# Optimization experiments

Measured on AMD Instinct MI355X. Metric: run time of the kernel, lower is better.

Reference implementation:

```python
import jax, jax.numpy as jnp
import numpy as np
from jax import lax

B, C, T, D, H, W = 1, 8, 8, 24, 48, 48
KT = 3  # temporal kernel taps (module's time loop == valid forward conv, stride 1, pad 0)
KS = 3  # spatial kernel size
S = 2   # spatial stride of the transposed conv
P = 1   # spatial padding of the transposed conv


def setup_inputs() -> dict:
    key = jax.random.key(0)
    kx, kw = jax.random.split(key)
    x = jax.random.normal(kx, (B, C, T, D, H, W), dtype=jnp.float32)
    # torch layout (out_channels, in_channels, kT, kD, kH, kW); the module assigns the
    # slice weight[:, :, i] directly as ConvTranspose3d.weight, so at runtime dim0 acts
    # as the transpose-conv INPUT-channel dim (works because in_ch == out_ch).
    fan_in = C * KT * KS ** 3
    bound = float(1.0 / np.sqrt(fan_in))
    weight = jax.random.uniform(kw, (C, C, KT, KS, KS, KS), dtype=jnp.float32,
                                minval=-bound, maxval=bound)
    return {"x": x, "weight": weight}


def _convT3d(x5, wt):
    # x5: [N, Cin, D, H, W]; wt: ConvTranspose3d weight laid out [Cin, Cout, kD, kH, kW].
    # Transposed conv == forward conv with spatially flipped kernel, swapped I/O dims,
    # lhs dilation = stride, per-side padding = dil*(k-1) - p.
    rhs = jnp.flip(wt, axis=(2, 3, 4)).transpose(1, 0, 2, 3, 4)  # [Cout, Cin, k, k, k]
    pad = KS - 1 - P
    return lax.conv_general_dilated(
        x5, rhs,
        window_strides=(1, 1, 1),
        padding=[(pad, pad)] * 3,
        lhs_dilation=(S, S, S),
        dimension_numbers=("NCDHW", "OIDHW", "NCDHW"))


def reference(x, weight):
    b, c, t = x.shape[:3]
    t_o = t - (KT - 1)  # temporal valid forward conv: out[f] = sum_i conv_i(x[f + i])
    # fold time into batch so each temporal tap is a single big 3D conv
    xr = x.transpose(0, 2, 1, 3, 4, 5).reshape(b * t, c, *x.shape[3:])
    out = None
    for i in range(KT):  # small fixed loop over kernel taps
        y = _convT3d(xr, weight[:, :, i])                 # [b*t, C, Do, Ho, Wo]
        y = y.reshape(b, t, *y.shape[1:])[:, i:i + t_o]   # frames x[f+i] -> out[f]
        out = y if out is None else out + y
    return out.transpose(0, 2, 1, 3, 4, 5)  # [B, C, t_o, Do, Ho, Wo]
```

## Files before the change

kernel.cpp:

```cpp
#include <hip/hip_runtime.h>


typedef float  f32x4  __attribute__((ext_vector_type(4)));
typedef float  f4a    __attribute__((ext_vector_type(4)));
typedef short  bf16x8 __attribute__((ext_vector_type(8)));
typedef unsigned int u32;
typedef u32    u32x2  __attribute__((ext_vector_type(2)));
typedef u32    u32x4  __attribute__((ext_vector_type(4)));

namespace {
constexpr int T_ = 8, D_ = 24, H_ = 48, W_ = 48;
constexpr int TO = 6, DO_ = 47, HO = 95, WO = 95;
constexpr int XCS = T_ * D_ * H_ * W_;
constexpr int XFS = D_ * H_ * W_;
constexpr int XDS = H_ * W_;
constexpr long OCS = (long)TO * DO_ * HO * WO;
constexpr int OFS = DO_ * HO * WO;
constexpr int ODS = HO * WO;

constexpr int AG[4] = {24, 12, 12, 8};
constexpr int AOFF[4] = {0, 3072, 4608, 6144};
constexpr int NRSTR = 146;

__global__ __launch_bounds__(256) void pack_kernel(const float* __restrict__ w,
                                                   unsigned short* __restrict__ A) {
  const int tid = blockIdx.x * 256 + threadIdx.x;
  const int nthr = gridDim.x * 256;
  const int KR[4] = {192, 96, 96, 48};
  for (int c = 0; c < 4; ++c) {
    const int cnt = AG[c] * 128;
    for (int e = tid; e < cnt; e += nthr) {
      const int j = e & 7, r = (e >> 3) & 15, g = e >> 7;
      const int k = g * 8 + j;
      float v = 0.f;
      if (k < KR[c]) {
        int gg = -1, kd = 1, kh = 1;
        const int cc = j & 1;
        if (c == 0)      { gg = g;               kd = ((j >> 1) & 1) ? 2 : 0; kh = ((j >> 2) & 1) ? 0 : 2; }
        else if (c == 1) { gg = 2 * g + (j >> 2); kd = ((j >> 1) & 1) ? 2 : 0; kh = 1; }
        else if (c == 2) { gg = 2 * g + (j >> 2); kd = 1; kh = ((j >> 1) & 1) ? 0 : 2; }
        else             { gg = 4 * g + (j >> 1); kd = 1; kh = 1; }
        if (gg >= 0 && gg < 24) {
          const int ci = gg / 3, i = gg - 3 * (gg / 3);
          const int co = r & 7;
          int kw = (r < 8) ? (cc == 0 ? 1 : -1) : (cc == 0 ? 2 : 0);
          if (kw >= 0) v = w[ci * 648 + co * 81 + i * 27 + kd * 9 + kh * 3 + kw];
        }
      }
      u32 u = __float_as_uint(v);
      u += 0x7FFFu + ((u >> 16) & 1u);
      A[AOFF[c] + e] = (unsigned short)(u >> 16);
    }
  }
}

template<int PD, int PH>
__device__ __forceinline__ void wave_body(
    const u32* __restrict__ lds, const unsigned short* __restrict__ A,
    float* __restrict__ out, int f, int od, int oh, int ihb, int lane)
{
  constexpr int CLS = (PD && PH) ? 0 : PD ? 1 : PH ? 2 : 3;
  constexpr int NSTEP = (CLS == 0) ? 6 : (CLS == 3) ? 2 : 3;
  const int c15 = lane & 15, q = lane >> 4;
  const int th = ((oh + PH) >> 1) - ihb;

  bf16x8 af[NSTEP];
  {
    const unsigned short* Ap = A + AOFF[CLS] + c15 * 8;
    #pragma unroll
    for (int s = 0; s < NSTEP; ++s)
      af[s] = *reinterpret_cast<const bf16x8*>(Ap + (s * 4 + q) * 128);
  }

  f32x4 acc[3];
  #pragma unroll
  for (int b = 0; b < 3; ++b) acc[b] = {0, 0, 0, 0};

  #pragma unroll
  for (int blk = 0; blk < 3; ++blk) {
    const int n = blk * 16 + c15;
    const u32* col = lds + n * NRSTR;
    #pragma unroll
    for (int s = 0; s < NSTEP; ++s) {
      const int G = s * 4 + q;
      u32x4 ue;
      if constexpr (CLS == 0) {
        const u32* b = col + G * 6 + 2 * th - 2;
        const u32x2 lo = *reinterpret_cast<const u32x2*>(b);
        const u32x2 hi = *reinterpret_cast<const u32x2*>(b + 2);
        ue = u32x4{lo.x, lo.y, hi.x, hi.y};
      } else if constexpr (CLS == 1) {
        const u32* b = col + 2 * G * 6 + 2 * th;
        const u32x2 lo = *reinterpret_cast<const u32x2*>(b);
        const u32x2 hi = *reinterpret_cast<const u32x2*>(b + 6);
        ue = u32x4{lo.x, lo.y, hi.x, hi.y};
      } else if constexpr (CLS == 2) {
        const u32* b = col + 2 * G * 6 + 2 * th - 1;
        ue = u32x4{b[0], b[2], b[6], b[8]};
      } else {
        const int g4 = (G > 5) ? 20 : 4 * G;
        const u32* b = col + g4 * 6 + 2 * th + 1;
        ue = u32x4{b[0], b[6], b[12], b[18]};
      }
      acc[blk] = __builtin_amdgcn_mfma_f32_16x16x32_bf16(af[s], __builtin_bit_cast(bf16x8, ue), acc[blk], 0, 0, 0);
    }
  }

  const int isO = (q >= 2);
  const int co0 = (q & 1) * 4;
  #pragma unroll
  for (int blk = 0; blk < 3; ++blk) {
    const int ow = blk * 32 + 2 * c15 + isO;
    if (ow < 95) {
      const long ob = (long)f * OFS + (long)od * ODS + (long)oh * HO + ow;
      #pragma unroll
      for (int j = 0; j < 4; ++j)
        out[(long)(co0 + j) * OCS + ob] = acc[blk][j];
    }
  }
}

constexpr int NBLK = 6 * 24 * 24;

__global__ __launch_bounds__(512) void convt4d_kernel(
    const float* __restrict__ x, const unsigned short* __restrict__ A,
    float* __restrict__ out)
{
  __shared__ u32 lds[48 * NRSTR];

  constexpr int qq = NBLK / 8;
  const int bid = blockIdx.x;
  const int L = (bid & 7) * qq + (bid >> 3);
  const int og = L % 24;
  const int rest = L / 24;
  const int odp = rest % 24, f = rest / 24;

  const int tid = threadIdx.x;
  const int ihb = og * 2;
  const int idp = odp + 1;

  for (int c = tid; c < 144 * 12; c += 512) {
    const int row = c / 12, ch = c % 12;
    const int gg = row / 6;
    const int rem = row % 6;
    const int t = rem >> 1, e = rem & 1;
    const int i = gg % 3, ci = gg / 3;
    int plane = idp - e; if (plane > 23) plane = 23;
    int ih = ihb + t; if (ih > 47) ih = 47;
    const float* src = x + ci * XCS + (f + i) * XFS + plane * XDS + ih * W_ + ch * 4;
    const f4a v = *reinterpret_cast<const f4a*>(src);
    const float v4 = (ch == 11) ? 0.f : src[4];
    const u32 b0 = __float_as_uint(v.x), b1 = __float_as_uint(v.y);
    const u32 b2 = __float_as_uint(v.z), b3 = __float_as_uint(v.w);
    const u32 b4 = __float_as_uint(v4);
    u32* dst = lds + (4 * ch) * NRSTR + row;
    dst[0 * NRSTR] = __builtin_amdgcn_perm(b1, b0, 0x07060302u);
    dst[1 * NRSTR] = __builtin_amdgcn_perm(b2, b1, 0x07060302u);
    dst[2 * NRSTR] = __builtin_amdgcn_perm(b3, b2, 0x07060302u);
    dst[3 * NRSTR] = __builtin_amdgcn_perm(b4, b3, 0x07060302u);
  }
  __syncthreads();

  const int w = tid >> 6, lane = tid & 63;
  const int half = w >> 2;
  const int od = 2 * odp + half;
  if (od > 46) return;
  int oh = og * 4 + (w & 3);
  if (oh > 94) oh = 93;
  if (half) {
    if (oh & 1) wave_body<1, 1>(lds, A, out, f, od, oh, ihb, lane);
    else        wave_body<1, 0>(lds, A, out, f, od, oh, ihb, lane);
  } else {
    if (oh & 1) wave_body<0, 1>(lds, A, out, f, od, oh, ihb, lane);
    else        wave_body<0, 0>(lds, A, out, f, od, oh, ihb, lane);
  }
}
}

extern "C" void kernel_launch(void* const* d_in, const int* in_sizes, int n_in,
                              void* d_out, int out_size, void* d_ws, size_t ws_size,
                              hipStream_t stream) {
  const float* x = (const float*)d_in[0];
  const float* w = (const float*)d_in[1];
  float* out = (float*)d_out;
  unsigned short* A = (unsigned short*)d_ws;
  hipLaunchKernelGGL(pack_kernel, dim3(8), dim3(256), 0, stream, w, A);
  hipLaunchKernelGGL(convt4d_kernel, dim3(NBLK), dim3(512), 0, stream, x, A, out);
}
```

Baseline: 35.73 us.

## Compute two output frames per block to reuse staged input frames in LDS

Each block now produces two consecutive output time frames. It stages 4 input frames per channel in LDS (192 rows instead of 144), and the two frames share 2 of those staged input frames. The grid is halved and each wave keeps two accumulator sets. This cuts redundant global reads and LDS packing of overlapping temporal frames. In exchange it adds LDS per block, more registers and fewer blocks, which may lower occupancy and parallelism.

```diff
diff --git a/kernel.cpp b/kernel.cpp
--- a/kernel.cpp
+++ b/kernel.cpp
@@ -20,7 +20,7 @@
 
 constexpr int AG[4] = {24, 12, 12, 8};
 constexpr int AOFF[4] = {0, 3072, 4608, 6144};
-constexpr int NRSTR = 146;
+constexpr int NRSTR = 194;
 
 __global__ __launch_bounds__(256) void pack_kernel(const float* __restrict__ w,
                                                    unsigned short* __restrict__ A) {
@@ -54,10 +54,15 @@
   }
 }
 
+__device__ __forceinline__ int rowb(int gg, int dl) {
+  const int ci = gg / 3;
+  return (ci * 4 + (gg - 3 * ci) + dl) * 6;
+}
+
 template<int PD, int PH>
 __device__ __forceinline__ void wave_body(
     const u32* __restrict__ lds, const unsigned short* __restrict__ A,
-    float* __restrict__ out, int f, int od, int oh, int ihb, int lane)
+    float* __restrict__ out, int f0, int od, int oh, int ihb, int lane)
 {
   constexpr int CLS = (PD && PH) ? 0 : PD ? 1 : PH ? 2 : 3;
   constexpr int NSTEP = (CLS == 0) ? 6 : (CLS == 3) ? 2 : 3;
@@ -72,9 +77,11 @@
       af[s] = *reinterpret_cast<const bf16x8*>(Ap + (s * 4 + q) * 128);
   }
 
-  f32x4 acc[3];
+  f32x4 acc[2][3];
   #pragma unroll
-  for (int b = 0; b < 3; ++b) acc[b] = {0, 0, 0, 0};
+  for (int dl = 0; dl < 2; ++dl)
+    #pragma unroll
+    for (int b = 0; b < 3; ++b) acc[dl][b] = {0, 0, 0, 0};
 
   #pragma unroll
   for (int blk = 0; blk < 3; ++blk) {
@@ -83,44 +90,54 @@
     #pragma unroll
     for (int s = 0; s < NSTEP; ++s) {
       const int G = s * 4 + q;
-      u32x4 ue;
-      if constexpr (CLS == 0) {
-        const u32* b = col + G * 6 + 2 * th - 2;
-        const u32x2 lo = *reinterpret_cast<const u32x2*>(b);
-        const u32x2 hi = *reinterpret_cast<const u32x2*>(b + 2);
-        ue = u32x4{lo.x, lo.y, hi.x, hi.y};
-      } else if constexpr (CLS == 1) {
-        const u32* b = col + 2 * G * 6 + 2 * th;
-        const u32x2 lo = *reinterpret_cast<const u32x2*>(b);
-        const u32x2 hi = *reinterpret_cast<const u32x2*>(b + 6);
-        ue = u32x4{lo.x, lo.y, hi.x, hi.y};
-      } else if constexpr (CLS == 2) {
-        const u32* b = col + 2 * G * 6 + 2 * th - 1;
-        ue = u32x4{b[0], b[2], b[6], b[8]};
-      } else {
-        const int g4 = (G > 5) ? 20 : 4 * G;
-        const u32* b = col + g4 * 6 + 2 * th + 1;
-        ue = u32x4{b[0], b[6], b[12], b[18]};
+      #pragma unroll
+      for (int dl = 0; dl < 2; ++dl) {
+        u32x4 ue;
+        if constexpr (CLS == 0) {
+          const u32* b = col + rowb(G, dl) + 2 * th - 2;
+          const u32x2 lo = *reinterpret_cast<const u32x2*>(b);
+          const u32x2 hi = *reinterpret_cast<const u32x2*>(b + 2);
+          ue = u32x4{lo.x, lo.y, hi.x, hi.y};
+        } else if constexpr (CLS == 1) {
+          const u32* b0 = col + rowb(2 * G, dl) + 2 * th;
+          const u32* b1 = col + rowb(2 * G + 1, dl) + 2 * th;
+          const u32x2 lo = *reinterpret_cast<const u32x2*>(b0);
+          const u32x2 hi = *reinterpret_cast<const u32x2*>(b1);
+          ue = u32x4{lo.x, lo.y, hi.x, hi.y};
+        } else if constexpr (CLS == 2) {
+          const int r0 = rowb(2 * G, dl), r1 = rowb(2 * G + 1, dl);
+          ue = u32x4{col[r0 + 2 * th - 1], col[r0 + 2 * th + 1],
+                     col[r1 + 2 * th - 1], col[r1 + 2 * th + 1]};
+        } else {
+          #pragma unroll
+          for (int d = 0; d < 4; ++d) {
+            int gg = 4 * G + d; gg = (gg > 23) ? 23 : gg;
+            ue[d] = col[rowb(gg, dl) + 2 * th + 1];
+          }
+        }
+        acc[dl][blk] = __builtin_amdgcn_mfma_f32_16x16x32_bf16(af[s], __builtin_bit_cast(bf16x8, ue), acc[dl][blk], 0, 0, 0);
       }
-      acc[blk] = __builtin_amdgcn_mfma_f32_16x16x32_bf16(af[s], __builtin_bit_cast(bf16x8, ue), acc[blk], 0, 0, 0);
     }
   }
 
   const int isO = (q >= 2);
   const int co0 = (q & 1) * 4;
   #pragma unroll
-  for (int blk = 0; blk < 3; ++blk) {
-    const int ow = blk * 32 + 2 * c15 + isO;
-    if (ow < 95) {
-      const long ob = (long)f * OFS + (long)od * ODS + (long)oh * HO + ow;
-      #pragma unroll
-      for (int j = 0; j < 4; ++j)
-        out[(long)(co0 + j) * OCS + ob] = acc[blk][j];
+  for (int dl = 0; dl < 2; ++dl) {
+    #pragma unroll
+    for (int blk = 0; blk < 3; ++blk) {
+      const int ow = blk * 32 + 2 * c15 + isO;
+      if (ow < 95) {
+        const long ob = (long)(f0 + dl) * OFS + (long)od * ODS + (long)oh * HO + ow;
+        #pragma unroll
+        for (int j = 0; j < 4; ++j)
+          out[(long)(co0 + j) * OCS + ob] = acc[dl][blk][j];
+      }
     }
   }
 }
 
-constexpr int NBLK = 6 * 24 * 24;
+constexpr int NBLK = 3 * 24 * 24;
 
 __global__ __launch_bounds__(512) void convt4d_kernel(
     const float* __restrict__ x, const unsigned short* __restrict__ A,
@@ -133,21 +150,22 @@
   const int L = (bid & 7) * qq + (bid >> 3);
   const int og = L % 24;
   const int rest = L / 24;
-  const int odp = rest % 24, f = rest / 24;
+  const int odp = rest % 24, fp = rest / 24;
+  const int f0 = 2 * fp;
 
   const int tid = threadIdx.x;
   const int ihb = og * 2;
   const int idp = odp + 1;
 
-  for (int c = tid; c < 144 * 12; c += 512) {
+  for (int c = tid; c < 192 * 12; c += 512) {
     const int row = c / 12, ch = c % 12;
-    const int gg = row / 6;
+    const int ggp = row / 6;
     const int rem = row % 6;
     const int t = rem >> 1, e = rem & 1;
-    const int i = gg % 3, ci = gg / 3;
+    const int ci = ggp >> 2, fi = ggp & 3;
     int plane = idp - e; if (plane > 23) plane = 23;
     int ih = ihb + t; if (ih > 47) ih = 47;
-    const float* src = x + ci * XCS + (f + i) * XFS + plane * XDS + ih * W_ + ch * 4;
+    const float* src = x + ci * XCS + (f0 + fi) * XFS + plane * XDS + ih * W_ + ch * 4;
     const f4a v = *reinterpret_cast<const f4a*>(src);
     const float v4 = (ch == 11) ? 0.f : src[4];
     const u32 b0 = __float_as_uint(v.x), b1 = __float_as_uint(v.y);
@@ -168,11 +186,11 @@
   int oh = og * 4 + (w & 3);
   if (oh > 94) oh = 93;
   if (half) {
-    if (oh & 1) wave_body<1, 1>(lds, A, out, f, od, oh, ihb, lane);
-    else        wave_body<1, 0>(lds, A, out, f, od, oh, ihb, lane);
+    if (oh & 1) wave_body<1, 1>(lds, A, out, f0, od, oh, ihb, lane);
+    else        wave_body<1, 0>(lds, A, out, f0, od, oh, ihb, lane);
   } else {
-    if (oh & 1) wave_body<0, 1>(lds, A, out, f, od, oh, ihb, lane);
-    else        wave_body<0, 0>(lds, A, out, f, od, oh, ihb, lane);
+    if (oh & 1) wave_body<0, 1>(lds, A, out, f0, od, oh, ihb, lane);
+    else        wave_body<0, 0>(lds, A, out, f0, od, oh, ihb, lane);
   }
 }
 }
```

After: 33.37 us. -6.6%, faster.
